# Performance work log

Hardware: AMD Instinct MI355X
Metric: run time of the kernel (lower is better)

## Reference

```python
import jax, jax.numpy as jnp
import numpy as np

B0, C0, H0, W0 = 2, 64, 48, 48
BR, DI, NS, RK, K = 128, 128, 16, 4, 4
EPS = 1e-5


def _bn_relu(x, g, b):
    # eval-mode BatchNorm2d (running mean 0, var 1) followed by ReLU; x is NCHW
    return jax.nn.relu(x * (g / jnp.sqrt(1.0 + EPS))[None, :, None, None] + b[None, :, None, None])


def _c1(x, w):
    # 1x1 conv, w: (O, C, 1, 1)
    return jnp.einsum('bchw,oc->bohw', x, w[:, :, 0, 0])


def _avgpool(x, k, s, p):
    # torch AvgPool2d with count_include_pad=True -> divide by k*k
    y = jax.lax.reduce_window(x, 0.0, jax.lax.add, (1, 1, k, k), (1, 1, s, s), ((0, 0), (0, 0), (p, p), (p, p)))
    return y / float(k * k)


def _resize(x, h, w):
    # bilinear, align_corners=False (half-pixel), NCHW
    return jax.image.resize(x, (x.shape[0], x.shape[1], h, w), 'bilinear')


def _pappm(x, s0_g, s0_b, s0_w, s1_g, s1_b, s1_w, s2_g, s2_b, s2_w, s3_g, s3_b, s3_w, s4_g, s4_b, s4_w, comp_g, comp_b, comp_w, sc_g, sc_b, sc_w):
    h, w = x.shape[2], x.shape[3]
    x0 = _c1(_bn_relu(x, s0_g, s0_b), s0_w)
    y1 = _c1(_bn_relu(_avgpool(x, 3, 1, 1), s1_g, s1_b), s1_w) + x0  # stride-1 pool keeps size
    y2 = _resize(_c1(_bn_relu(_avgpool(x, 5, 2, 2), s2_g, s2_b), s2_w), h, w) + x0
    y3 = _resize(_c1(_bn_relu(_avgpool(x, 9, 4, 4), s3_g, s3_b), s3_w), h, w) + x0
    y4 = _c1(_bn_relu(x.mean((2, 3), keepdims=True), s4_g, s4_b), s4_w) + x0  # 1x1 -> broadcast
    cat = jnp.concatenate([x0, y1, y2, y3, y4], axis=1)  # (B, 5*BR, H, W)
    comp = jax.lax.conv_general_dilated(_bn_relu(cat, comp_g, comp_b), comp_w, (1, 1), ((1, 1), (1, 1)), dimension_numbers=('NCHW', 'OIHW', 'NCHW'))
    return comp + _c1(_bn_relu(x, sc_g, sc_b), sc_w)


def _ss2d(xin, in_proj_w, dw_w, dw_b, x_proj_w, dt_w, dt_b, A_logs, Ds, ln_g, ln_b, out_proj_w):
    # xin: (B, H, W, d_model)
    Bb, Hh, Ww, _ = xin.shape
    xz = xin @ in_proj_w.T                      # (B,H,W,2*DI)
    xc, z = jnp.split(xz, 2, axis=-1)
    xc = jnp.transpose(xc, (0, 3, 1, 2))        # (B,DI,H,W)
    xc = jax.lax.conv_general_dilated(xc, dw_w, (1, 1), ((1, 1), (1, 1)), dimension_numbers=('NCHW', 'OIHW', 'NCHW'), feature_group_count=DI)
    xc = jax.nn.silu(xc + dw_b[None, :, None, None])
    L = Hh * Ww
    x_hw = xc.reshape(Bb, DI, L)
    x_wh = jnp.transpose(xc, (0, 1, 3, 2)).reshape(Bb, DI, L)
    xs = jnp.stack([x_hw, x_wh, x_hw[:, :, ::-1], x_wh[:, :, ::-1]], axis=1)  # (B,K,DI,L)
    x_dbl = jnp.einsum('bkdl,kcd->bkcl', xs, x_proj_w)
    dts, Bm, Cm = jnp.split(x_dbl, [RK, RK + NS], axis=2)  # (B,K,RK,L),(B,K,NS,L),(B,K,NS,L)
    delta = jax.nn.softplus(jnp.einsum('bkrl,kdr->bkdl', dts, dt_w) + dt_b[None, :, :, None])  # (B,K,DI,L)
    A = -jnp.exp(A_logs).reshape(K, DI, NS)
    a = jnp.exp(delta[..., None] * A[None, :, :, None, :])                    # (B,K,DI,L,NS)
    bu = (delta * xs)[..., None] * jnp.transpose(Bm, (0, 1, 3, 2))[:, :, None]  # (B,K,DI,L,NS)

    def comb(e1, e2):
        a1, b1 = e1
        a2, b2 = e2
        return a2 * a1, a2 * b1 + b2

    _, hst = jax.lax.associative_scan(comb, (a, bu), axis=3)  # h_t = a_t*h_{t-1} + b_t
    y = jnp.einsum('bkdln,bknl->bkdl', hst, Cm) + xs * Ds.reshape(K, DI)[None, :, :, None]
    inv = y[:, 2:4][:, :, :, ::-1]
    y3 = jnp.transpose(y[:, 1].reshape(Bb, DI, Ww, Hh), (0, 1, 3, 2)).reshape(Bb, DI, L)
    y4 = jnp.transpose(inv[:, 1].reshape(Bb, DI, Ww, Hh), (0, 1, 3, 2)).reshape(Bb, DI, L)
    ys = jnp.transpose(y[:, 0] + inv[:, 0] + y3 + y4, (0, 2, 1)).reshape(Bb, Hh, Ww, DI)
    mu = ys.mean(-1, keepdims=True)
    var = jnp.mean((ys - mu) ** 2, -1, keepdims=True)
    yn = (ys - mu) / jnp.sqrt(var + EPS) * ln_g + ln_b
    return (yn * jax.nn.silu(z)) @ out_proj_w.T  # (B,H,W,d_model)


def setup_inputs():
    key = jax.random.key(0)
    ks = iter(jax.random.split(key, 32))
    nrm = lambda shp, s: jax.random.normal(next(ks), shp, jnp.float32) * s
    d = {}
    d['x'] = nrm((B0, C0, H0, W0), 1.0)
    for nm in ['s0', 's1', 's2', 's3', 's4']:
        d[nm + '_g'] = jnp.ones((C0,), jnp.float32)
        d[nm + '_b'] = jnp.zeros((C0,), jnp.float32)
        d[nm + '_w'] = nrm((BR, C0, 1, 1), (2.0 / C0) ** 0.5)
    d['comp_g'] = jnp.ones((5 * BR,), jnp.float32)
    d['comp_b'] = jnp.zeros((5 * BR,), jnp.float32)
    d['comp_w'] = nrm((C0, 5 * BR, 3, 3), (2.0 / (5 * BR * 9)) ** 0.5)
    d['sc_g'] = jnp.ones((C0,), jnp.float32)
    d['sc_b'] = jnp.zeros((C0,), jnp.float32)
    d['sc_w'] = nrm((C0, C0, 1, 1), (2.0 / C0) ** 0.5)
    d['in_proj_w'] = nrm((2 * DI, C0), C0 ** -0.5)
    d['dw_w'] = nrm((DI, 1, 3, 3), 0.3)
    d['dw_b'] = jnp.zeros((DI,), jnp.float32)
    d['x_proj_w'] = nrm((K, RK + 2 * NS, DI), DI ** -0.5)
    d['dt_w'] = nrm((K, DI, RK), RK ** -0.5)
    d['dt_b'] = jnp.log(jnp.expm1(jnp.asarray(0.01, jnp.float32))) * jnp.ones((K, DI), jnp.float32)
    d['A_logs'] = jnp.tile(jnp.log(jnp.arange(1, NS + 1, dtype=jnp.float32))[None], (K * DI, 1))
    d['Ds'] = jnp.ones((K * DI,), jnp.float32)
    d['ln_g'] = jnp.ones((DI,), jnp.float32)
    d['ln_b'] = jnp.zeros((DI,), jnp.float32)
    d['out_proj_w'] = nrm((C0, DI), DI ** -0.5)
    d['fc1_w'] = nrm((BR, C0, 1, 1), C0 ** -0.5)
    d['fc1_b'] = jnp.zeros((BR,), jnp.float32)
    d['fc2_w'] = nrm((C0, BR, 1, 1), BR ** -0.5)
    d['fc2_b'] = jnp.zeros((C0,), jnp.float32)
    return d


def reference(x, s0_g, s0_b, s0_w, s1_g, s1_b, s1_w, s2_g, s2_b, s2_w, s3_g, s3_b, s3_w, s4_g, s4_b, s4_w, comp_g, comp_b, comp_w, sc_g, sc_b, sc_w, in_proj_w, dw_w, dw_b, x_proj_w, dt_w, dt_b, A_logs, Ds, ln_g, ln_b, out_proj_w, fc1_w, fc1_b, fc2_w, fc2_b):
    p = _pappm(x, s0_g, s0_b, s0_w, s1_g, s1_b, s1_w, s2_g, s2_b, s2_w, s3_g, s3_b, s3_w, s4_g, s4_b, s4_w, comp_g, comp_b, comp_w, sc_g, sc_b, sc_w)
    a = _ss2d(jnp.transpose(p, (0, 2, 3, 1)), in_proj_w, dw_w, dw_b, x_proj_w, dt_w, dt_b, A_logs, Ds, ln_g, ln_b, out_proj_w)
    x1 = jnp.transpose(a, (0, 3, 1, 2))  # (B,C0,H,W)
    h1 = jax.nn.silu(_c1(x1, fc1_w) + fc1_b[None, :, None, None])
    return _c1(h1, fc2_w) + fc2_b[None, :, None, None] + x1
```

## Files before the change

kernel.cpp:

```cpp
#include <hip/hip_runtime.h>
#include <math.h>

constexpr int cB = 2, cC = 64, cH = 48, cW = 48, cL = 48 * 48;
constexpr int cBR = 128, cDI = 128, cNS = 16, cRK = 4, cK = 4;
constexpr float cEPS = 1e-5f;
constexpr int NCH = 32;
constexpr int CHL = cL / NCH;
constexpr int KTOT = 5824;

typedef unsigned short u16;
typedef unsigned int u32;
typedef short s16x8 __attribute__((ext_vector_type(8)));
typedef float f32x4 __attribute__((ext_vector_type(4)));

__device__ __forceinline__ float bnrelu(float v, float g, float b) {
    float y = v * (g * rsqrtf(1.0f + cEPS)) + b;
    return y > 0.f ? y : 0.f;
}
__device__ __forceinline__ float silu(float v) {
    return v / (1.f + __expf(-v));
}
__device__ __forceinline__ u16 f2bf(float f) {
    u32 u = __float_as_uint(f);
    u = (u + 0x7fffu + ((u >> 16) & 1u)) >> 16;
    return (u16)u;
}
__device__ __forceinline__ s16x8 cvt8(const float* p) {
    s16x8 r;
#pragma unroll
    for (int i = 0; i < 8; i++) r[i] = (short)f2bf(p[i]);
    return r;
}
__device__ __forceinline__ float row_sum16(float v) {
    v += __int_as_float(__builtin_amdgcn_update_dpp(0, __float_as_int(v), 0xB1, 0xF, 0xF, true));
    v += __int_as_float(__builtin_amdgcn_update_dpp(0, __float_as_int(v), 0x4E, 0xF, 0xF, true));
    v += __int_as_float(__builtin_amdgcn_update_dpp(0, __float_as_int(v), 0x124, 0xF, 0xF, true));
    v += __int_as_float(__builtin_amdgcn_update_dpp(0, __float_as_int(v), 0x128, 0xF, 0xF, true));
    return v;
}

__global__ void __launch_bounds__(256) k_pp(const float* __restrict__ x,
                                            float* __restrict__ pool5, float* __restrict__ pool9,
                                            float* __restrict__ gmean,
                                            const float* __restrict__ cw, const float* __restrict__ scw,
                                            const float* __restrict__ s0w, const float* __restrict__ s1w,
                                            const float* __restrict__ ipw, const float* __restrict__ xpw,
                                            const float* __restrict__ dww,
                                            const float* __restrict__ s2w, const float* __restrict__ s3w,
                                            u16* __restrict__ w8, u16* __restrict__ wcat,
                                            u16* __restrict__ ipk, u16* __restrict__ xpk,
                                            float* __restrict__ dwk, u16* __restrict__ c1k) {
    __shared__ float sm[4];
    int blk = blockIdx.x;
    int t = threadIdx.x;
    if (blk < 288) {
        int idx = blk * 256 + t;
        int w = idx % 24, h = (idx / 24) % 24, bc = idx / 576;
        const float* p = x + bc * cL;
        float s = 0.f;
        for (int kh = 0; kh < 5; kh++) {
            int hh = h * 2 - 2 + kh; if (hh < 0 || hh >= cH) continue;
            for (int kw = 0; kw < 5; kw++) {
                int ww = w * 2 - 2 + kw; if (ww < 0 || ww >= cW) continue;
                s += p[hh * cW + ww];
            }
        }
        pool5[idx] = s * (1.f / 25.f);
    } else if (blk < 360) {
        int idx = (blk - 288) * 256 + t;
        int w = idx % 12, h = (idx / 12) % 12, bc = idx / 144;
        const float* p = x + bc * cL;
        float s = 0.f;
        for (int kh = 0; kh < 9; kh++) {
            int hh = h * 4 - 4 + kh; if (hh < 0 || hh >= cH) continue;
            for (int kw = 0; kw < 9; kw++) {
                int ww = w * 4 - 4 + kw; if (ww < 0 || ww >= cW) continue;
                s += p[hh * cW + ww];
            }
        }
        pool9[idx] = s * (1.f / 81.f);
    } else if (blk < 488) {
        int bc = blk - 360;
        const float* p = x + bc * cL;
        float s = 0.f;
        for (int i = t; i < cL; i += 256) s += p[i];
        for (int m = 32; m > 0; m >>= 1) s += __shfl_down(s, m);
        if ((t & 63) == 0) sm[t >> 6] = s;
        __syncthreads();
        if (t == 0) gmean[bc] = (sm[0] + sm[1] + sm[2] + sm[3]) * (1.f / cL);
    } else if (blk < 1944) {
        int idx = (blk - 488) * 256 + t;
        int o = idx / KTOT, kx = idx % KTOT;
        float v;
        if (kx < 5760) { int tap = kx / 640, ch = kx % 640; v = cw[(o * 640 + ch) * 9 + tap]; }
        else v = scw[o * 64 + (kx - 5760)];
        w8[(((size_t)(kx >> 3) * 64) + o) * 8 + (kx & 7)] = f2bf(v);
    } else if (blk < 2008) {
        int idx = (blk - 1944) * 256 + t;
        int g = idx >> 13, r = idx & 8191;
        int o = r >> 6, c = r & 63;
        float v = (g ? s1w : s0w)[r];
        int kt = c >> 5, q = (c >> 3) & 3, j = c & 7, nt = o >> 4, ln = o & 15;
        wcat[(size_t)((((g * 2 + kt) * 4 + q) * 8 + nt) * 16 + ln) * 8 + j] = f2bf(v);
    } else if (blk < 2072) {
        int idx = (blk - 2008) * 256 + t;
        int o = idx >> 6, c = idx & 63;
        int kt = c >> 5, q = (c >> 3) & 3, j = c & 7, nt = o >> 4, ln = o & 15;
        ipk[(size_t)(((kt * 4 + q) * 16 + nt) * 16 + ln) * 8 + j] = f2bf(ipw[idx]);
    } else if (blk < 2144) {
        int idx = (blk - 2072) * 256 + t;
        int o = idx >> 7, d = idx & 127;
        int kt = d >> 5, q = (d >> 3) & 3, j = d & 7, nt = o >> 4, ln = o & 15;
        xpk[(size_t)(((kt * 4 + q) * 9 + nt) * 16 + ln) * 8 + j] = f2bf(xpw[idx]);
    } else if (blk < 2149) {
        int idx = (blk - 2144) * 256 + t;
        if (idx < 1152) {
            int tap = idx >> 7, ch = idx & 127;
            dwk[idx] = dww[ch * 9 + tap];
        }
    } else {
        int idx = (blk - 2149) * 256 + t;
        int g = idx >> 13, r = idx & 8191;
        int o = r >> 6, c = r & 63;
        float v = (g ? s3w : s2w)[r];
        int kt = c >> 5, q = (c >> 3) & 3, j = c & 7, nt = o >> 4, ln = o & 15;
        c1k[(size_t)((((g * 2 + kt) * 4 + q) * 8 + nt) * 16 + ln) * 8 + j] = f2bf(v);
    }
}

__global__ void __launch_bounds__(256) k_c1m(const float* __restrict__ pool5, const float* __restrict__ pool9,
                                             const float* __restrict__ gm,
                                             const float* __restrict__ s2g, const float* __restrict__ s2b,
                                             const float* __restrict__ s3g, const float* __restrict__ s3b,
                                             const float* __restrict__ s4g, const float* __restrict__ s4b,
                                             const float* __restrict__ s4w, const u16* __restrict__ c1k,
                                             float* __restrict__ c2cl, float* __restrict__ c3cl,
                                             float* __restrict__ c4) {
    int blk = blockIdx.x, t = threadIdx.x;
    if (blk >= 90) {
        int b = blk - 90;
        __shared__ float v[64];
        if (t < 64) v[t] = bnrelu(gm[b * 64 + t], s4g[t], s4b[t]);
        __syncthreads();
        if (t < 128) {
            const float* wr = s4w + t * 64;
            float acc = 0.f;
#pragma unroll 16
            for (int c = 0; c < 64; c++) acc += v[c] * wr[c];
            c4[b * 128 + t] = acc;
        }
        return;
    }
    int set, b, pp0, HW;
    const float *in, *g, *bb;
    float* outp;
    if (blk < 72) { set = 0; b = blk / 36; pp0 = (blk % 36) * 16; HW = 576; in = pool5; g = s2g; bb = s2b; outp = c2cl + (size_t)b * 576 * 128; }
    else { int r = blk - 72; set = 1; b = r / 9; pp0 = (r % 9) * 16; HW = 144; in = pool9; g = s3g; bb = s3b; outp = c3cl + (size_t)b * 144 * 128; }
    __shared__ u16 av16[16][72];
#pragma unroll
    for (int i = 0; i < 4; i++) {
        int id = i * 256 + t;
        int c = id >> 4, p = id & 15;
        av16[p][c] = f2bf(bnrelu(in[(size_t)(b * 64 + c) * HW + pp0 + p], g[c], bb[c]));
    }
    __syncthreads();
    int wv = t >> 6, lane = t & 63, ln = lane & 15, q = lane >> 4;
    f32x4 acc[2] = {};
#pragma unroll
    for (int kt = 0; kt < 2; kt++) {
        s16x8 a = *(const s16x8*)(&av16[ln][kt * 32 + q * 8]);
#pragma unroll
        for (int jn = 0; jn < 2; jn++) {
            int nt = wv * 2 + jn;
            s16x8 bfr = *(const s16x8*)(c1k + (size_t)((((set * 2 + kt) * 4 + q) * 8 + nt) * 16 + ln) * 8);
            acc[jn] = __builtin_amdgcn_mfma_f32_16x16x32_bf16(a, bfr, acc[jn], 0, 0, 0);
        }
    }
#pragma unroll
    for (int jn = 0; jn < 2; jn++) {
        int o = (wv * 2 + jn) * 16 + ln;
#pragma unroll
        for (int r = 0; r < 4; r++)
            outp[(size_t)(pp0 + q * 4 + r) * 128 + o] = acc[jn][r];
    }
}

__global__ void __launch_bounds__(512) k_cat2(
    const float* __restrict__ x, const float* __restrict__ c4,
    const float* __restrict__ s0g, const float* __restrict__ s0b,
    const float* __restrict__ s1g, const float* __restrict__ s1b,
    const float* __restrict__ scg, const float* __restrict__ scb,
    const float* __restrict__ cg, const float* __restrict__ cbb,
    const u16* __restrict__ wcat, const float* __restrict__ c2cl, const float* __restrict__ c3cl,
    u16* __restrict__ catbf, u16* __restrict__ xbf) {
    int blk = blockIdx.x;
    int b = blk / 144;
    int l0 = (blk % 144) * 16;
    int hrow = l0 / cW, w0g = l0 % cW;
    int t = threadIdx.x;
    __shared__ float xst[64][3][19];
    __shared__ float axv[16][68];
    __shared__ float ap3[16][68];
    __shared__ u16 axc[16][66];
#pragma unroll
    for (int i = 0; i < 7; i++) {
        int id = i * 512 + t;
        if (id < 3456) {
            int c = id / 54, rem = id % 54, rw = rem / 18, wi = rem % 18;
            int hh = hrow + rw - 1, ww = w0g + wi - 1;
            float v = 0.f;
            if (hh >= 0 && hh < cH && ww >= 0 && ww < cW)
                v = x[(size_t)(b * 64 + c) * cL + hh * cW + ww];
            xst[c][rw][wi] = v;
        }
    }
    __syncthreads();
#pragma unroll
    for (int i = 0; i < 2; i++) {
        int id = i * 512 + t;
        int c = id >> 4, p = id & 15;
        float xv = xst[c][1][p + 1];
        float s9 = 0.f;
#pragma unroll
        for (int rw = 0; rw < 3; rw++)
#pragma unroll
            for (int wi = 0; wi < 3; wi++)
                s9 += xst[c][rw][p + wi];
        axv[p][c] = bnrelu(xv, s0g[c], s0b[c]);
        ap3[p][c] = bnrelu(s9 * (1.f / 9.f), s1g[c], s1b[c]);
        axc[p][c] = f2bf(bnrelu(xv, scg[c], scb[c]));
    }
    __syncthreads();
#pragma unroll
    for (int i = 0; i < 2; i++) {
        int idx = i * 512 + t;
        int pp = idx >> 6, cc = idx & 63;
        xbf[((size_t)b * cL + l0 + pp) * 64 + cc] = axc[pp][cc];
    }
    int wv = t >> 6, lane = t & 63, ln = lane & 15, q = lane >> 4;
    f32x4 ax = {};
    f32x4 ay = {};
#pragma unroll
    for (int kt = 0; kt < 2; kt++) {
        s16x8 a0 = cvt8(&axv[ln][kt * 32 + q * 8]);
        s16x8 a1 = cvt8(&ap3[ln][kt * 32 + q * 8]);
        s16x8 b0 = *(const s16x8*)(wcat + (size_t)((((0 * 2 + kt) * 4 + q) * 8 + wv) * 16 + ln) * 8);
        s16x8 b1 = *(const s16x8*)(wcat + (size_t)((((1 * 2 + kt) * 4 + q) * 8 + wv) * 16 + ln) * 8);
        ax = __builtin_amdgcn_mfma_f32_16x16x32_bf16(a0, b0, ax, 0, 0, 0);
        ay = __builtin_amdgcn_mfma_f32_16x16x32_bf16(a1, b1, ay, 0, 0, 0);
    }
    float sy2 = hrow * 0.5f - 0.25f;
    float fy2 = floorf(sy2); int iy2 = (int)fy2; float ay2 = sy2 - fy2;
    int y20 = min(max(iy2, 0), 23), y21 = min(max(iy2 + 1, 0), 23);
    float sy3 = hrow * 0.25f - 0.375f;
    float fy3 = floorf(sy3); int iy3 = (int)fy3; float ay3 = sy3 - fy3;
    int y30 = min(max(iy3, 0), 11), y31 = min(max(iy3 + 1, 0), 11);
    const float* c2b = c2cl + (size_t)b * 576 * 128;
    const float* c3b = c3cl + (size_t)b * 144 * 128;
    int ch = wv * 16 + ln;
    float c4v = c4[b * 128 + ch];
#pragma unroll
    for (int r = 0; r < 4; r++) {
        int pp = q * 4 + r;
        int wq = w0g + pp;
        float sx2 = wq * 0.5f - 0.25f;
        float fx2 = floorf(sx2); int ix2 = (int)fx2; float ax2 = sx2 - fx2;
        int x20 = min(max(ix2, 0), 23), x21 = min(max(ix2 + 1, 0), 23);
        float sx3 = wq * 0.25f - 0.375f;
        float fx3 = floorf(sx3); int ix3 = (int)fx3; float ax3 = sx3 - fx3;
        int x30 = min(max(ix3, 0), 11), x31 = min(max(ix3 + 1, 0), 11);
        float v00 = c2b[(y20 * 24 + x20) * 128 + ch], v01 = c2b[(y20 * 24 + x21) * 128 + ch];
        float v10 = c2b[(y21 * 24 + x20) * 128 + ch], v11 = c2b[(y21 * 24 + x21) * 128 + ch];
        float t0 = v00 + (v01 - v00) * ax2, t1 = v10 + (v11 - v10) * ax2;
        float u2v = t0 + (t1 - t0) * ay2;
        float w00 = c3b[(y30 * 12 + x30) * 128 + ch], w01 = c3b[(y30 * 12 + x31) * 128 + ch];
        float w10 = c3b[(y31 * 12 + x30) * 128 + ch], w11 = c3b[(y31 * 12 + x31) * 128 + ch];
        float s0_ = w00 + (w01 - w00) * ax3, s1_ = w10 + (w11 - w10) * ax3;
        float u3v = s0_ + (s1_ - s0_) * ay3;
        float x0 = ax[r];
        float y1 = ay[r] + x0;
        float y2 = x0 + u2v;
        float y3 = x0 + u3v;
        float y4 = x0 + c4v;
        u16* base = catbf + ((size_t)b * cL + l0 + pp) * 640;
        base[ch]       = f2bf(bnrelu(x0, cg[ch],       cbb[ch]));
        base[128 + ch] = f2bf(bnrelu(y1, cg[128 + ch], cbb[128 + ch]));
        base[256 + ch] = f2bf(bnrelu(y2, cg[256 + ch], cbb[256 + ch]));
        base[384 + ch] = f2bf(bnrelu(y3, cg[384 + ch], cbb[384 + ch]));
        base[512 + ch] = f2bf(bnrelu(y4, cg[512 + ch], cbb[512 + ch]));
    }
}

__global__ void __launch_bounds__(512) k_compip(const u16* __restrict__ catbf,
                                                const u16* __restrict__ xbf,
                                                const u16* __restrict__ w8,
                                                const u16* __restrict__ ipk,
                                                float* __restrict__ xc, float* __restrict__ z) {
    int pix0 = blockIdx.x * 16;
    int b = pix0 / cL;
    int t = threadIdx.x;
    int wv = t >> 6, lane = t & 63, ln = lane & 15, q = lane >> 4;
    __shared__ float pl[8][16][68];
    __shared__ u16 pv16[16][72];
    int la = (pix0 + ln) - b * cL;
    int h = la / cW, w = la % cW;
    f32x4 acc[4] = {};
    int ks0 = wv * 23;
    int kcnt = (wv == 7) ? 21 : 23;
    for (int i = 0; i < kcnt; i++) {
        int ks = ks0 + i;
        s16x8 av;
        if (ks < 180) {
            int s = ks / 20;
            int cc = ks - s * 20;
            int s3 = s / 3;
            int kh = s3 - 1, kw = s - s3 * 3 - 1;
            int hh = h + kh, ww = w + kw;
            bool ok = (hh >= 0) && (hh < cH) && (ww >= 0) && (ww < cW);
            const u16* ap = catbf + (((size_t)b * cL + hh * cW + ww) * 640 + cc * 32 + q * 8);
            if (ok) av = *(const s16x8*)ap;
            else av = s16x8{0, 0, 0, 0, 0, 0, 0, 0};
        } else {
            int cc = ks - 180;
            av = *(const s16x8*)(xbf + (size_t)(pix0 + ln) * 64 + cc * 32 + q * 8);
        }
        const u16* wrow = w8 + ((size_t)ks * 4 + q) * 512;
#pragma unroll
        for (int j = 0; j < 4; j++) {
            s16x8 bv = *(const s16x8*)(wrow + (size_t)(j * 16 + ln) * 8);
            acc[j] = __builtin_amdgcn_mfma_f32_16x16x32_bf16(av, bv, acc[j], 0, 0, 0);
        }
    }
#pragma unroll
    for (int j = 0; j < 4; j++)
#pragma unroll
        for (int r = 0; r < 4; r++)
            pl[wv][q * 4 + r][j * 16 + ln] = acc[j][r];
    __syncthreads();
#pragma unroll
    for (int e = 0; e < 2; e++) {
        int id = e * 512 + t;
        int p = id >> 6, c = id & 63;
        float s = 0.f;
#pragma unroll
        for (int w2 = 0; w2 < 8; w2++) s += pl[w2][p][c];
        pv16[p][c] = f2bf(s);
    }
    __syncthreads();
    f32x4 a2[2] = {};
#pragma unroll
    for (int kt = 0; kt < 2; kt++) {
        s16x8 a = *(const s16x8*)(&pv16[ln][kt * 32 + q * 8]);
#pragma unroll
        for (int jn = 0; jn < 2; jn++) {
            int nt = wv * 2 + jn;
            s16x8 bfr = *(const s16x8*)(ipk + (size_t)(((kt * 4 + q) * 16 + nt) * 16 + ln) * 8);
            a2[jn] = __builtin_amdgcn_mfma_f32_16x16x32_bf16(a, bfr, a2[jn], 0, 0, 0);
        }
    }
#pragma unroll
    for (int jn = 0; jn < 2; jn++) {
        int o = (wv * 2 + jn) * 16 + ln;
#pragma unroll
        for (int r = 0; r < 4; r++) {
            int p = q * 4 + r;
            if (o < 128) xc[((size_t)pix0 + p) * 128 + o] = a2[jn][r];
            else         z[((size_t)pix0 + p) * 128 + (o - 128)] = a2[jn][r];
        }
    }
}

__global__ void __launch_bounds__(1024) k_xdbl4(const float* __restrict__ xc, const float* __restrict__ dwk,
                                                const float* __restrict__ dwb,
                                                const u16* __restrict__ xpk,
                                                const float* __restrict__ dtw, const float* __restrict__ dtb,
                                                float* __restrict__ bc, float* __restrict__ delta,
                                                float* __restrict__ xca) {
    int blk = blockIdx.x;
    int b = blk / 144;
    int l0 = (blk % 144) * 16;
    int hrow = l0 / cW, w0 = l0 % cW;
    int t = threadIdx.x;
    __shared__ float hal[3][18][128];
    __shared__ float av[16][132];
    __shared__ float Dt[16][148];
#pragma unroll
    for (int i = 0; i < 7; i++) {
        int id = i * 1024 + t;
        if (id < 6912) {
            int d = id & 127;
            int rem = id >> 7;
            int wi = rem % 18, rw = rem / 18;
            int hh = hrow + rw - 1, ww = w0 + wi - 1;
            float v = 0.f;
            if (hh >= 0 && hh < cH && ww >= 0 && ww < cW)
                v = xc[((size_t)b * cL + hh * cW + ww) * 128 + d];
            hal[rw][wi][d] = v;
        }
    }
    __syncthreads();
#pragma unroll
    for (int i = 0; i < 2; i++) {
        int id = i * 1024 + t;
        int d = id & 127, p = id >> 7;
        float acc = dwb[d];
#pragma unroll
        for (int rw = 0; rw < 3; rw++)
#pragma unroll
            for (int wi = 0; wi < 3; wi++)
                acc += hal[rw][p + wi][d] * dwk[(rw * 3 + wi) * 128 + d];
        float v = silu(acc);
        av[p][d] = v;
        xca[((size_t)b * cL + l0 + p) * 128 + d] = v;
    }
    __syncthreads();
    int wv = t >> 6, lane = t & 63, ln = lane & 15, q = lane >> 4;
    if (wv < 9) {
        int nt = wv;
        f32x4 acc = {};
#pragma unroll
        for (int kt = 0; kt < 4; kt++) {
            s16x8 a = cvt8(&av[ln][kt * 32 + q * 8]);
            s16x8 bfr = *(const s16x8*)(xpk + (size_t)(((kt * 4 + q) * 9 + nt) * 16 + ln) * 8);
            acc = __builtin_amdgcn_mfma_f32_16x16x32_bf16(a, bfr, acc, 0, 0, 0);
        }
#pragma unroll
        for (int r = 0; r < 4; r++)
            Dt[q * 4 + r][nt * 16 + ln] = acc[r];
    }
    __syncthreads();
#pragma unroll
    for (int i = 0; i < 2; i++) {
        int id = i * 1024 + t;
        int cc = id & 31, kk = (id >> 5) & 3, p = id >> 7;
        bc[((size_t)(b * 4 + kk) * cL + l0 + p) * 32 + cc] = Dt[p][kk * 36 + 4 + cc];
    }
    {
        int d = t & 127;
        int kk = (t >> 7) & 3;
        int p0 = t >> 9;
        const float* wd = dtw + (size_t)(kk * 128 + d) * 4;
        float w0_ = wd[0], w1 = wd[1], w2 = wd[2], w3 = wd[3];
        float bb = dtb[kk * 128 + d];
        float* dout = delta + ((size_t)(b * 4 + kk) * cL + l0) * 128 + d;
#pragma unroll
        for (int i = 0; i < 8; i++) {
            int p = p0 + i * 2;
            float pre = bb + w0_ * Dt[p][kk * 36] + w1 * Dt[p][kk * 36 + 1]
                      + w2 * Dt[p][kk * 36 + 2] + w3 * Dt[p][kk * 36 + 3];
            float dl = pre > 20.f ? pre : __logf(1.f + __expf(pre));
            dout[(size_t)p * 128] = dl;
        }
    }
}

__device__ __forceinline__ int xs_index(int k, int l) {
    int lp = (k & 2) ? (cL - 1 - l) : l;
    if (k & 1) { int w = lp / cH, h = lp % cH; return h * cW + w; }
    return lp;
}

__global__ void __launch_bounds__(256) k_scan1(const float* __restrict__ delta, const float* __restrict__ xca,
                                               const float* __restrict__ bc, const float* __restrict__ Alogs,
                                               float* __restrict__ Pend, float* __restrict__ hend) {
    int blk = blockIdx.x;
    int c = blk & 31;
    if (c == NCH - 1) return;
    int g = blk >> 5;
    int dgq = g & 7, bk = g >> 3;
    int k = bk & 3, b = bk >> 2;
    int t = threadIdx.x;
    int n = t & 15;
    int dq = t >> 4;
    int d0 = dgq * 16;
    __shared__ int soff[CHL];
    __shared__ float sdl[CHL][16];
    __shared__ float sxv[CHL][16];
    __shared__ float sbp[CHL][16];
    if (t < CHL) soff[t] = xs_index(k, c * CHL + t);
    __syncthreads();
    const float* dp = delta + (size_t)bk * cL * 128 + d0;
    const float* xp = xca + (size_t)b * cL * 128 + d0;
    const float* bcp = bc + (size_t)bk * cL * 32;
#pragma unroll
    for (int e = 0; e < 5; e++) {
        int idx = e * 256 + t;
        if (idx < CHL * 16) {
            int i = idx >> 4, j = idx & 15;
            int off = soff[i];
            sdl[i][j] = dp[(size_t)off * 128 + j];
            sxv[i][j] = xp[(size_t)off * 128 + j];
            sbp[i][j] = bcp[(size_t)off * 32 + j];
        }
    }
    __syncthreads();
    float A = -__expf(Alogs[(k * 128 + d0 + dq) * 16 + n]);
    float P = 1.f, h = 0.f;
#pragma unroll 8
    for (int i = 0; i < CHL; i++) {
        float dl = sdl[i][dq];
        float a = __expf(dl * A);
        h = a * h + dl * sxv[i][dq] * sbp[i][n];
        P *= a;
    }
    Pend[(size_t)blk * 256 + t] = P;
    hend[(size_t)blk * 256 + t] = h;
}

__global__ void __launch_bounds__(256) k_scan3(const float* __restrict__ delta, const float* __restrict__ xca,
                                               const float* __restrict__ bc, const float* __restrict__ Alogs,
                                               const float* __restrict__ Dsv,
                                               const float* __restrict__ Pend, const float* __restrict__ hend,
                                               float* __restrict__ y) {
    int blk = blockIdx.x;
    int c = blk & 31;
    int g = blk >> 5;
    int dgq = g & 7, bk = g >> 3;
    int k = bk & 3, b = bk >> 2;
    int t = threadIdx.x;
    int n = t & 15;
    int dq = t >> 4;
    int d0 = dgq * 16;
    __shared__ int soff[CHL];
    __shared__ float sdl[CHL][16];
    __shared__ float sxv[CHL][16];
    __shared__ float sbc[CHL][32];
    if (t < CHL) soff[t] = xs_index(k, c * CHL + t);
    __syncthreads();
    const float* dp = delta + (size_t)bk * cL * 128 + d0;
    const float* xp = xca + (size_t)b * cL * 128 + d0;
    const float* bcp = bc + (size_t)bk * cL * 32;
#pragma unroll
    for (int e = 0; e < 5; e++) {
        int idx = e * 256 + t;
        if (idx < CHL * 16) {
            int i = idx >> 4, j = idx & 15;
            int off = soff[i];
            sdl[i][j] = dp[(size_t)off * 128 + j];
            sxv[i][j] = xp[(size_t)off * 128 + j];
        }
    }
#pragma unroll
    for (int e = 0; e < 9; e++) {
        int idx = e * 256 + t;
        if (idx < CHL * 32) {
            int i = idx >> 5, j = idx & 31;
            sbc[i][j] = bcp[(size_t)soff[i] * 32 + j];
        }
    }
    float h = 0.f;
    for (int cc = 0; cc < c; cc++) {
        size_t idx = ((size_t)g * NCH + cc) * 256 + t;
        h = Pend[idx] * h + hend[idx];
    }
    __syncthreads();
    float A = -__expf(Alogs[(k * 128 + d0 + dq) * 16 + n]);
    float Dsd = Dsv[k * 128 + d0 + dq];
    float* yb = y + (size_t)bk * cL * 128 + d0 + dq;
#pragma unroll 8
    for (int i = 0; i < CHL; i++) {
        float dl = sdl[i][dq];
        float xv = sxv[i][dq];
        float a = __expf(dl * A);
        h = a * h + dl * xv * sbc[i][n];
        float contrib = row_sum16(h * sbc[i][16 + n]);
        if (n == 0) yb[(size_t)soff[i] * 128] = contrib + xv * Dsd;
    }
}

__global__ void __launch_bounds__(256) k_tail(const float* __restrict__ y, const float* __restrict__ z,
                                              const float* __restrict__ lng, const float* __restrict__ lnb,
                                              const float* __restrict__ opw,
                                              const float* __restrict__ f1w, const float* __restrict__ f1b,
                                              const float* __restrict__ f2w, const float* __restrict__ f2b,
                                              float* __restrict__ out) {
    int blk = blockIdx.x;
    int b = blk / 576;
    int l0 = (blk % 576) * 4;
    int t = threadIdx.x;
    __shared__ float v[4][132];
    __shared__ float x1s[4][68];
    __shared__ float h1s[4][132];
    __shared__ float mus[4], rss[4];
    const float* yb = y + (size_t)b * 4 * cL * 128;
#pragma unroll
    for (int i = 0; i < 2; i++) {
        int id = i * 256 + t;
        int d = id & 127, p = id >> 7;
        size_t base = (size_t)(l0 + p) * 128 + d;
        v[p][d] = yb[base] + yb[(size_t)cL * 128 + base] + yb[(size_t)2 * cL * 128 + base] + yb[(size_t)3 * cL * 128 + base];
    }
    __syncthreads();
    if (t < 64) {
        int p = t >> 4, c8 = (t & 15) * 8;
        float s = 0.f;
#pragma unroll
        for (int j = 0; j < 8; j++) s += v[p][c8 + j];
        s = row_sum16(s);
        float mu = s * (1.f / 128.f);
        float s2 = 0.f;
#pragma unroll
        for (int j = 0; j < 8; j++) { float dv = v[p][c8 + j] - mu; s2 += dv * dv; }
        s2 = row_sum16(s2);
        if ((t & 15) == 0) { mus[p] = mu; rss[p] = rsqrtf(s2 * (1.f / 128.f) + cEPS); }
    }
    __syncthreads();
#pragma unroll
    for (int i = 0; i < 2; i++) {
        int id = i * 256 + t;
        int d = id & 127, p = id >> 7;
        float zz = z[((size_t)b * cL + l0 + p) * 128 + d];
        v[p][d] = ((v[p][d] - mus[p]) * rss[p] * lng[d] + lnb[d]) * silu(zz);
    }
    __syncthreads();
    {
        int p = t & 3, o = t >> 2;
        const float* wr = opw + o * 128;
        float acc = 0.f;
#pragma unroll 16
        for (int d2 = 0; d2 < 128; d2++) acc += v[p][d2] * wr[d2];
        x1s[p][o] = acc;
    }
    __syncthreads();
#pragma unroll
    for (int i = 0; i < 2; i++) {
        int id = i * 256 + t;
        int p = id & 3, j = id >> 2;
        const float* wr = f1w + j * 64;
        float acc = f1b[j];
#pragma unroll 16
        for (int c = 0; c < 64; c++) acc += x1s[p][c] * wr[c];
        h1s[p][j] = silu(acc);
    }
    __syncthreads();
    {
        int p = t & 3, o = t >> 2;
        const float* wr = f2w + o * 128;
        float acc = f2b[o];
#pragma unroll 16
        for (int j = 0; j < 128; j++) acc += h1s[p][j] * wr[j];
        out[((size_t)b * 64 + o) * cL + l0 + p] = acc + x1s[p][o];
    }
}

extern "C" void kernel_launch(void* const* d_in, const int* in_sizes, int n_in,
                              void* d_out, int out_size, void* d_ws, size_t ws_size,
                              hipStream_t stream) {
    (void)in_sizes; (void)n_in; (void)out_size; (void)ws_size;
    const float* x    = (const float*)d_in[0];
    const float* s0g  = (const float*)d_in[1];
    const float* s0b  = (const float*)d_in[2];
    const float* s0w  = (const float*)d_in[3];
    const float* s1g  = (const float*)d_in[4];
    const float* s1b  = (const float*)d_in[5];
    const float* s1w  = (const float*)d_in[6];
    const float* s2g  = (const float*)d_in[7];
    const float* s2b  = (const float*)d_in[8];
    const float* s2w  = (const float*)d_in[9];
    const float* s3g  = (const float*)d_in[10];
    const float* s3b  = (const float*)d_in[11];
    const float* s3w  = (const float*)d_in[12];
    const float* s4g  = (const float*)d_in[13];
    const float* s4b  = (const float*)d_in[14];
    const float* s4w  = (const float*)d_in[15];
    const float* cg   = (const float*)d_in[16];
    const float* cbb  = (const float*)d_in[17];
    const float* cw   = (const float*)d_in[18];
    const float* scg  = (const float*)d_in[19];
    const float* scb  = (const float*)d_in[20];
    const float* scw  = (const float*)d_in[21];
    const float* ipw  = (const float*)d_in[22];
    const float* dww  = (const float*)d_in[23];
    const float* dwb  = (const float*)d_in[24];
    const float* xpw  = (const float*)d_in[25];
    const float* dtw  = (const float*)d_in[26];
    const float* dtb  = (const float*)d_in[27];
    const float* Alog = (const float*)d_in[28];
    const float* Dsv  = (const float*)d_in[29];
    const float* lng  = (const float*)d_in[30];
    const float* lnb  = (const float*)d_in[31];
    const float* opw  = (const float*)d_in[32];
    const float* f1w  = (const float*)d_in[33];
    const float* f1b  = (const float*)d_in[34];
    const float* f2w  = (const float*)d_in[35];
    const float* f2b  = (const float*)d_in[36];
    float* out = (float*)d_out;

    float* ws = (float*)d_ws;
    size_t off = 0;
    float* pool5  = ws + off; off += 73728;
    float* pool9  = ws + off; off += 18432;
    float* gmean  = ws + off; off += 128;
    float* c2cl   = ws + off; off += 147456;
    float* c3cl   = ws + off; off += 36864;
    float* c4     = ws + off; off += 256;
    u16*   catbf  = (u16*)(ws + off); off += 1474560;
    u16*   xbf    = (u16*)(ws + off); off += 147456;
    u16*   w8     = (u16*)(ws + off); off += 186368;
    u16*   wcat   = (u16*)(ws + off); off += 8192;
    u16*   ipk    = (u16*)(ws + off); off += 8192;
    u16*   c1k    = (u16*)(ws + off); off += 8192;
    if (off < 2359296) off = 2359296;
    float* xc     = ws + off; off += 589824;
    u16*   xpk    = (u16*)(ws + off); off += 9216;
    float* dwk    = ws + off; off += 1280;
    float* xca    = ws + off; off += 589824;
    float* zbuf   = ws + off; off += 589824;
    float* bcbuf  = ws + off; off += 589824;
    float* Pend   = ws + off; off += 524288;
    float* ybuf   = ws + off; off += 2359296;
    off += 294912;
    float* delta  = ws + 0;
    float* hend   = xc;

    k_pp<<<2213, 256, 0, stream>>>(x, pool5, pool9, gmean,
                                   cw, scw, s0w, s1w, ipw, xpw, dww, s2w, s3w,
                                   w8, wcat, ipk, xpk, dwk, c1k);
    k_c1m<<<92, 256, 0, stream>>>(pool5, pool9, gmean, s2g, s2b, s3g, s3b, s4g, s4b, s4w,
                                  c1k, c2cl, c3cl, c4);
    k_cat2<<<cB * 144, 512, 0, stream>>>(x, c4, s0g, s0b, s1g, s1b, scg, scb, cg, cbb,
                                         wcat, c2cl, c3cl, catbf, xbf);
    k_compip<<<cB * cL / 16, 512, 0, stream>>>(catbf, xbf, w8, ipk, xc, zbuf);
    k_xdbl4<<<cB * 144, 1024, 0, stream>>>(xc, dwk, dwb, xpk, dtw, dtb, bcbuf, delta, xca);
    k_scan1<<<64 * NCH, 256, 0, stream>>>(delta, xca, bcbuf, Alog, Pend, hend);
    k_scan3<<<64 * NCH, 256, 0, stream>>>(delta, xca, bcbuf, Alog, Dsv, Pend, hend, ybuf);
    k_tail<<<cB * 576, 256, 0, stream>>>(ybuf, zbuf, lng, lnb, opw, f1w, f1b, f2w, f2b, out);
}
```

Baseline: 255.3 us.

## Merge chunked scan passes into one kernel with a grid-wide atomic barrier

```diff
diff --git a/kernel.cpp b/kernel.cpp
--- a/kernel.cpp
+++ b/kernel.cpp
@@ -7,6 +7,7 @@
 constexpr int NCH = 32;
 constexpr int CHL = cL / NCH;
 constexpr int KTOT = 5824;
+constexpr unsigned int SCAN_BLOCKS = 64 * NCH;
 
 typedef unsigned short u16;
 typedef unsigned int u32;
@@ -460,58 +461,11 @@
     return lp;
 }
 
-__global__ void __launch_bounds__(256) k_scan1(const float* __restrict__ delta, const float* __restrict__ xca,
-                                               const float* __restrict__ bc, const float* __restrict__ Alogs,
-                                               float* __restrict__ Pend, float* __restrict__ hend) {
-    int blk = blockIdx.x;
-    int c = blk & 31;
-    if (c == NCH - 1) return;
-    int g = blk >> 5;
-    int dgq = g & 7, bk = g >> 3;
-    int k = bk & 3, b = bk >> 2;
-    int t = threadIdx.x;
-    int n = t & 15;
-    int dq = t >> 4;
-    int d0 = dgq * 16;
-    __shared__ int soff[CHL];
-    __shared__ float sdl[CHL][16];
-    __shared__ float sxv[CHL][16];
-    __shared__ float sbp[CHL][16];
-    if (t < CHL) soff[t] = xs_index(k, c * CHL + t);
-    __syncthreads();
-    const float* dp = delta + (size_t)bk * cL * 128 + d0;
-    const float* xp = xca + (size_t)b * cL * 128 + d0;
-    const float* bcp = bc + (size_t)bk * cL * 32;
-#pragma unroll
-    for (int e = 0; e < 5; e++) {
-        int idx = e * 256 + t;
-        if (idx < CHL * 16) {
-            int i = idx >> 4, j = idx & 15;
-            int off = soff[i];
-            sdl[i][j] = dp[(size_t)off * 128 + j];
-            sxv[i][j] = xp[(size_t)off * 128 + j];
-            sbp[i][j] = bcp[(size_t)off * 32 + j];
-        }
-    }
-    __syncthreads();
-    float A = -__expf(Alogs[(k * 128 + d0 + dq) * 16 + n]);
-    float P = 1.f, h = 0.f;
-#pragma unroll 8
-    for (int i = 0; i < CHL; i++) {
-        float dl = sdl[i][dq];
-        float a = __expf(dl * A);
-        h = a * h + dl * sxv[i][dq] * sbp[i][n];
-        P *= a;
-    }
-    Pend[(size_t)blk * 256 + t] = P;
-    hend[(size_t)blk * 256 + t] = h;
-}
-
-__global__ void __launch_bounds__(256) k_scan3(const float* __restrict__ delta, const float* __restrict__ xca,
-                                               const float* __restrict__ bc, const float* __restrict__ Alogs,
-                                               const float* __restrict__ Dsv,
-                                               const float* __restrict__ Pend, const float* __restrict__ hend,
-                                               float* __restrict__ y) {
+__global__ void __launch_bounds__(256, 8) k_scanM(const float* __restrict__ delta, const float* __restrict__ xca,
+                                                  const float* __restrict__ bc, const float* __restrict__ Alogs,
+                                                  const float* __restrict__ Dsv,
+                                                  float* __restrict__ Pend, float* __restrict__ hend,
+                                                  float* __restrict__ y, u32* __restrict__ ctr) {
     int blk = blockIdx.x;
     int c = blk & 31;
     int g = blk >> 5;
@@ -548,13 +502,37 @@
             sbc[i][j] = bcp[(size_t)soff[i] * 32 + j];
         }
     }
+    __syncthreads();
+    float A = -__expf(Alogs[(k * 128 + d0 + dq) * 16 + n]);
+    if (c != NCH - 1) {
+        float P = 1.f, h1 = 0.f;
+#pragma unroll 8
+        for (int i = 0; i < CHL; i++) {
+            float dl = sdl[i][dq];
+            float a = __expf(dl * A);
+            h1 = a * h1 + dl * sxv[i][dq] * sbc[i][n];
+            P *= a;
+        }
+        Pend[(size_t)blk * 256 + t] = P;
+        hend[(size_t)blk * 256 + t] = h1;
+    }
+    __threadfence();
+    __syncthreads();
+    if (t == 0) {
+        __hip_atomic_fetch_add(ctr, 1u, __ATOMIC_ACQ_REL, __HIP_MEMORY_SCOPE_AGENT);
+        unsigned spins = 0;
+        while (__hip_atomic_load(ctr, __ATOMIC_ACQUIRE, __HIP_MEMORY_SCOPE_AGENT) < SCAN_BLOCKS) {
+            __builtin_amdgcn_s_sleep(8);
+            if (++spins > (1u << 24)) break;
+        }
+    }
+    __syncthreads();
+    __threadfence();
     float h = 0.f;
     for (int cc = 0; cc < c; cc++) {
         size_t idx = ((size_t)g * NCH + cc) * 256 + t;
         h = Pend[idx] * h + hend[idx];
     }
-    __syncthreads();
-    float A = -__expf(Alogs[(k * 128 + d0 + dq) * 16 + n]);
     float Dsd = Dsv[k * 128 + d0 + dq];
     float* yb = y + (size_t)bk * cL * 128 + d0 + dq;
 #pragma unroll 8
@@ -708,6 +686,7 @@
     float* zbuf   = ws + off; off += 589824;
     float* bcbuf  = ws + off; off += 589824;
     float* Pend   = ws + off; off += 524288;
+    u32*   scnt   = (u32*)(ws + off); off += 64;
     float* ybuf   = ws + off; off += 2359296;
     off += 294912;
     float* delta  = ws + 0;
@@ -722,7 +701,7 @@
                                          wcat, c2cl, c3cl, catbf, xbf);
     k_compip<<<cB * cL / 16, 512, 0, stream>>>(catbf, xbf, w8, ipk, xc, zbuf);
     k_xdbl4<<<cB * 144, 1024, 0, stream>>>(xc, dwk, dwb, xpk, dtw, dtb, bcbuf, delta, xca);
-    k_scan1<<<64 * NCH, 256, 0, stream>>>(delta, xca, bcbuf, Alog, Pend, hend);
-    k_scan3<<<64 * NCH, 256, 0, stream>>>(delta, xca, bcbuf, Alog, Dsv, Pend, hend, ybuf);
+    hipMemsetAsync(scnt, 0, sizeof(u32), stream);
+    k_scanM<<<SCAN_BLOCKS, 256, 0, stream>>>(delta, xca, bcbuf, Alog, Dsv, Pend, hend, ybuf, scnt);
     k_tail<<<cB * 576, 256, 0, stream>>>(ybuf, zbuf, lng, lnb, opw, f1w, f1b, f2w, f2b, out);
 }
```

Result: slower. 610.1 us (+139.0%).
